# Performance work log

Measured on AMD Instinct MI355X. Metric: run time of the kernel, lower is better.

The kernel has to match this reference:

```python
import jax, jax.numpy as jnp
import numpy as np

NUM_CEPS = 13  # default num_ceps in log_mel_to_cepstral


def _dct_basis(n_mels, num_ceps):
    # Orthonormal DCT-II basis (scipy.fftpack.dct type=2, norm='ortho'),
    # truncated to the first num_ceps rows. Shape (num_ceps, n_mels).
    n = jnp.arange(n_mels, dtype=jnp.float32)
    k = jnp.arange(num_ceps, dtype=jnp.float32)
    basis = jnp.cos(jnp.pi * (n[None, :] + 0.5) * k[:, None] / n_mels)
    scale = jnp.where(k == 0, jnp.sqrt(1.0 / n_mels), jnp.sqrt(2.0 / n_mels))
    return basis * scale[:, None]


def _log_mel_to_cepstral(mel, basis):
    # mel: (B, 1, F, T) -> cepstral (B, num_ceps, T) with CMVN over (B*T)
    x = jnp.log1p(jnp.abs(mel[:, 0]))                 # (B, F, T)
    c = jnp.einsum('kf,bft->bkt', basis, x)           # (B, num_ceps, T)
    mean = jnp.mean(c, axis=(0, 2), keepdims=True)
    # torch .std is unbiased (ddof=1) over the B*T flattened samples
    std = jnp.std(c, axis=(0, 2), keepdims=True, ddof=1) + 1e-6
    return (c - mean) / std


def setup_inputs() -> dict:
    key = jax.random.key(0)
    k1, k2 = jax.random.split(key)
    B, F, T = 64, 128, 4096
    mel_true = jax.random.normal(k1, (B, 1, F, T), dtype=jnp.float32)
    mel_pred = jax.random.normal(k2, (B, 1, F, T), dtype=jnp.float32)
    return {"mel_true": mel_true, "mel_pred": mel_pred}


def reference(mel_true, mel_pred):
    n_mels = mel_true.shape[2]
    basis = _dct_basis(n_mels, NUM_CEPS)
    c_true = _log_mel_to_cepstral(mel_true, basis)
    c_pred = _log_mel_to_cepstral(mel_pred, basis)
    diff = c_true - c_pred
    mse_dist = jnp.sum(diff * diff, axis=1)           # (B, T)
    log_base_10 = 10.0 / jnp.log(jnp.float32(10.0))
    mcd = log_base_10 * jnp.sqrt(2.0 * mse_dist)
    return jnp.mean(mcd)
```

## Files before the change

### kernel.cpp

```cpp
#include <hip/hip_runtime.h>
#include <math.h>

#define BB 64
#define FF 128
#define TT 4096
#define KK 13
#define NT (BB * TT)
#define NP (NT / 2)
#define SCALE0 0.08838834764831845f
#define SCALEK 0.125f
#define MCD_C  6.14185100f

#define KLIST(X) X(0) X(1) X(2) X(3) X(4) X(5) X(6) X(7) X(8) X(9) X(10) X(11) X(12)
#define K12(X)        X(1) X(2) X(3) X(4) X(5) X(6) X(7) X(8) X(9) X(10) X(11) X(12)

__global__ __launch_bounds__(256, 2) void pass1_kernel(
    const float* __restrict__ melT, const float* __restrict__ melP,
    float* __restrict__ sums, float* __restrict__ cT, float* __restrict__ cP)
{
    const int gp = blockIdx.x * 256 + threadIdx.x;
    const int g0 = gp << 1;
    const int b  = g0 >> 12;
    const int t0 = g0 & (TT - 1);
    const float* pT = melT + (size_t)b * FF * TT + t0;
    const float* pP = melP + (size_t)b * FF * TT + t0;

#define DECLACC(i) float tx##i = 0.f, ty##i = 0.f, px##i = 0.f, py##i = 0.f;
    KLIST(DECLACC)

#pragma unroll 4
    for (int f = 0; f < FF; ++f) {
        const float2 vT = *(const float2*)(pT + (size_t)f * TT);
        const float2 vP = *(const float2*)(pP + (size_t)f * TT);
        float xTx = __logf(1.0f + fabsf(vT.x));
        float xTy = __logf(1.0f + fabsf(vT.y));
        float xPx = __logf(1.0f + fabsf(vP.x));
        float xPy = __logf(1.0f + fabsf(vP.y));

        float b1 = __cosf((3.14159265358979f / 128.0f) * ((float)f + 0.5f));
        float tw = b1 + b1;
        float b2  = fmaf(tw, b1,  -1.0f);
        float b3  = fmaf(tw, b2,  -b1);
        float b4  = fmaf(tw, b3,  -b2);
        float b5  = fmaf(tw, b4,  -b3);
        float b6  = fmaf(tw, b5,  -b4);
        float b7  = fmaf(tw, b6,  -b5);
        float b8  = fmaf(tw, b7,  -b6);
        float b9  = fmaf(tw, b8,  -b7);
        float b10 = fmaf(tw, b9,  -b8);
        float b11 = fmaf(tw, b10, -b9);
        float b12 = fmaf(tw, b11, -b10);

        tx0 += xTx; ty0 += xTy; px0 += xPx; py0 += xPy;
#define FMAK(i) tx##i = fmaf(b##i, xTx, tx##i); ty##i = fmaf(b##i, xTy, ty##i); \
                px##i = fmaf(b##i, xPx, px##i); py##i = fmaf(b##i, xPy, py##i);
        K12(FMAK)
#undef FMAK
    }

    tx0 *= SCALE0; ty0 *= SCALE0; px0 *= SCALE0; py0 *= SCALE0;
#define SCK(i) tx##i *= SCALEK; ty##i *= SCALEK; px##i *= SCALEK; py##i *= SCALEK;
    K12(SCK)
#undef SCK

#define STK(i) { ((float2*)(cT + (size_t)(i) * NT))[gp] = make_float2(tx##i, ty##i); \
                 ((float2*)(cP + (size_t)(i) * NT))[gp] = make_float2(px##i, py##i); }
    KLIST(STK)
#undef STK

    __shared__ float red[4][52];
    const int lane = threadIdx.x & 63;
    const int wave = threadIdx.x >> 6;
#define REDK(i) { \
        float s1 = tx##i + ty##i; \
        float s2 = fmaf(tx##i, tx##i, ty##i * ty##i); \
        float s3 = px##i + py##i; \
        float s4 = fmaf(px##i, px##i, py##i * py##i); \
        for (int o = 32; o > 0; o >>= 1) { \
            s1 += __shfl_down(s1, o); s2 += __shfl_down(s2, o); \
            s3 += __shfl_down(s3, o); s4 += __shfl_down(s4, o); } \
        if (lane == 0) { red[wave][i] = s1; red[wave][13 + i] = s2; \
                         red[wave][26 + i] = s3; red[wave][39 + i] = s4; } }
    KLIST(REDK)
#undef REDK
    __syncthreads();
    if (threadIdx.x < 52) {
        atomicAdd(&sums[threadIdx.x],
                  red[0][threadIdx.x] + red[1][threadIdx.x] +
                  red[2][threadIdx.x] + red[3][threadIdx.x]);
    }
}

__global__ __launch_bounds__(256, 2) void pass2_kernel(
    const float* __restrict__ sums, const float* __restrict__ cT,
    const float* __restrict__ cP, float* __restrict__ out)
{
    __shared__ float mT[13], iT[13], mP[13], iP[13];
    if (threadIdx.x < 26) {
        const int arr = threadIdx.x >= 13;
        const int k   = threadIdx.x - arr * 13;
        const float s = sums[arr * 26 + k];
        const float q = sums[arr * 26 + 13 + k];
        const float N = (float)NT;
        const float m = s / N;
        const float var = fmaxf((q - s * m) / (N - 1.0f), 0.0f);
        const float isd = 1.0f / (sqrtf(var) + 1e-6f);
        if (arr == 0) { mT[k] = m; iT[k] = isd; }
        else          { mP[k] = m; iP[k] = isd; }
    }
    __syncthreads();

    const int gp = blockIdx.x * 256 + threadIdx.x;
    float ssx = 0.0f, ssy = 0.0f;
#pragma unroll
    for (int k = 0; k < KK; ++k) {
        const float2 a = ((const float2*)(cT + (size_t)k * NT))[gp];
        const float2 p = ((const float2*)(cP + (size_t)k * NT))[gp];
        const float dx = (a.x - mT[k]) * iT[k] - (p.x - mP[k]) * iP[k];
        const float dy = (a.y - mT[k]) * iT[k] - (p.y - mP[k]) * iP[k];
        ssx = fmaf(dx, dx, ssx);
        ssy = fmaf(dy, dy, ssy);
    }
    float v = MCD_C * (sqrtf(ssx) + sqrtf(ssy));

    const int lane = threadIdx.x & 63;
    const int wave = threadIdx.x >> 6;
    for (int o = 32; o > 0; o >>= 1) v += __shfl_down(v, o);
    __shared__ float r2[4];
    if (lane == 0) r2[wave] = v;
    __syncthreads();
    if (threadIdx.x == 0) {
        atomicAdd(out, (r2[0] + r2[1] + r2[2] + r2[3]) * (1.0f / (float)NT));
    }
}

extern "C" void kernel_launch(void* const* d_in, const int* in_sizes, int n_in,
                              void* d_out, int out_size, void* d_ws, size_t ws_size,
                              hipStream_t stream) {
    const float* melT = (const float*)d_in[0];
    const float* melP = (const float*)d_in[1];
    float* out  = (float*)d_out;
    float* sums = (float*)d_ws;
    float* cT   = (float*)((char*)d_ws + 256);
    float* cP   = cT + (size_t)KK * NT;

    hipMemsetAsync(d_ws, 0, 256, stream);
    hipMemsetAsync(d_out, 0, out_size * sizeof(float), stream);

    pass1_kernel<<<NP / 256, 256, 0, stream>>>(melT, melP, sums, cT, cP);
    pass2_kernel<<<NP / 256, 256, 0, stream>>>(sums, cT, cP, out);
}
```

Before: 296.5 us.

## Split pass1 per tensor, pad atomic sums, replace final atomic with reduce kernel

Pass1 now launches twice as many blocks, each handling only one of the two mel tensors. This halves the accumulator registers per thread and raises the launch-bounds occupancy target from 2 to 4 blocks per SM. The statistic sums are padded to 64-byte spacing to reduce atomic contention on shared cache lines. The final reduction writes per-block partials and adds a third single-block kernel in place of the global atomic, at the cost of an extra launch.

Measured after the change: 291.6 us. Within noise of the previous version (-1.7%).

```diff
diff --git a/kernel.cpp b/kernel.cpp
--- a/kernel.cpp
+++ b/kernel.cpp
@@ -6,106 +6,102 @@
 #define TT 4096
 #define KK 13
 #define NT (BB * TT)
-#define NP (NT / 2)
+#define NPAIR (NT / 2)
 #define SCALE0 0.08838834764831845f
 #define SCALEK 0.125f
 #define MCD_C  6.14185100f
 
+
 #define KLIST(X) X(0) X(1) X(2) X(3) X(4) X(5) X(6) X(7) X(8) X(9) X(10) X(11) X(12)
 #define K12(X)        X(1) X(2) X(3) X(4) X(5) X(6) X(7) X(8) X(9) X(10) X(11) X(12)
 
-__global__ __launch_bounds__(256, 2) void pass1_kernel(
+__global__ __launch_bounds__(256, 4) void pass1_kernel(
     const float* __restrict__ melT, const float* __restrict__ melP,
     float* __restrict__ sums, float* __restrict__ cT, float* __restrict__ cP)
 {
-    const int gp = blockIdx.x * 256 + threadIdx.x;
+    const int tensor = blockIdx.x >> 9;
+    const int gp = ((blockIdx.x & 511) << 8) + threadIdx.x;
+    const float* __restrict__ src = tensor ? melP : melT;
+    float* __restrict__ dst = tensor ? cP : cT;
+
     const int g0 = gp << 1;
     const int b  = g0 >> 12;
     const int t0 = g0 & (TT - 1);
-    const float* pT = melT + (size_t)b * FF * TT + t0;
-    const float* pP = melP + (size_t)b * FF * TT + t0;
+    const float* p = src + (size_t)b * (FF * TT) + t0;
 
-#define DECLACC(i) float tx##i = 0.f, ty##i = 0.f, px##i = 0.f, py##i = 0.f;
+#define DECLACC(i) float ax##i = 0.f, ay##i = 0.f;
     KLIST(DECLACC)
+#undef DECLACC
 
 #pragma unroll 4
     for (int f = 0; f < FF; ++f) {
-        const float2 vT = *(const float2*)(pT + (size_t)f * TT);
-        const float2 vP = *(const float2*)(pP + (size_t)f * TT);
-        float xTx = __logf(1.0f + fabsf(vT.x));
-        float xTy = __logf(1.0f + fabsf(vT.y));
-        float xPx = __logf(1.0f + fabsf(vP.x));
-        float xPy = __logf(1.0f + fabsf(vP.y));
+        const float2 v = *(const float2*)(p + (size_t)f * TT);
+        const float xx = __logf(1.0f + fabsf(v.x));
+        const float xy = __logf(1.0f + fabsf(v.y));
 
-        float b1 = __cosf((3.14159265358979f / 128.0f) * ((float)f + 0.5f));
-        float tw = b1 + b1;
-        float b2  = fmaf(tw, b1,  -1.0f);
-        float b3  = fmaf(tw, b2,  -b1);
-        float b4  = fmaf(tw, b3,  -b2);
-        float b5  = fmaf(tw, b4,  -b3);
-        float b6  = fmaf(tw, b5,  -b4);
-        float b7  = fmaf(tw, b6,  -b5);
-        float b8  = fmaf(tw, b7,  -b6);
-        float b9  = fmaf(tw, b8,  -b7);
-        float b10 = fmaf(tw, b9,  -b8);
-        float b11 = fmaf(tw, b10, -b9);
-        float b12 = fmaf(tw, b11, -b10);
+        const float b1 = __cosf((3.14159265358979f / 128.0f) * ((float)f + 0.5f));
+        const float tw = b1 + b1;
+        const float b2  = fmaf(tw, b1,  -1.0f);
+        const float b3  = fmaf(tw, b2,  -b1);
+        const float b4  = fmaf(tw, b3,  -b2);
+        const float b5  = fmaf(tw, b4,  -b3);
+        const float b6  = fmaf(tw, b5,  -b4);
+        const float b7  = fmaf(tw, b6,  -b5);
+        const float b8  = fmaf(tw, b7,  -b6);
+        const float b9  = fmaf(tw, b8,  -b7);
+        const float b10 = fmaf(tw, b9,  -b8);
+        const float b11 = fmaf(tw, b10, -b9);
+        const float b12 = fmaf(tw, b11, -b10);
 
-        tx0 += xTx; ty0 += xTy; px0 += xPx; py0 += xPy;
-#define FMAK(i) tx##i = fmaf(b##i, xTx, tx##i); ty##i = fmaf(b##i, xTy, ty##i); \
-                px##i = fmaf(b##i, xPx, px##i); py##i = fmaf(b##i, xPy, py##i);
+        ax0 += xx; ay0 += xy;
+#define FMAK(i) ax##i = fmaf(b##i, xx, ax##i); ay##i = fmaf(b##i, xy, ay##i);
         K12(FMAK)
 #undef FMAK
     }
 
-    tx0 *= SCALE0; ty0 *= SCALE0; px0 *= SCALE0; py0 *= SCALE0;
-#define SCK(i) tx##i *= SCALEK; ty##i *= SCALEK; px##i *= SCALEK; py##i *= SCALEK;
+    ax0 *= SCALE0; ay0 *= SCALE0;
+#define SCK(i) ax##i *= SCALEK; ay##i *= SCALEK;
     K12(SCK)
 #undef SCK
 
-#define STK(i) { ((float2*)(cT + (size_t)(i) * NT))[gp] = make_float2(tx##i, ty##i); \
-                 ((float2*)(cP + (size_t)(i) * NT))[gp] = make_float2(px##i, py##i); }
+#define STK(i) ((float2*)(dst + (size_t)(i) * NT))[gp] = make_float2(ax##i, ay##i);
     KLIST(STK)
 #undef STK
 
-    __shared__ float red[4][52];
+    __shared__ float red[4][26];
     const int lane = threadIdx.x & 63;
     const int wave = threadIdx.x >> 6;
 #define REDK(i) { \
-        float s1 = tx##i + ty##i; \
-        float s2 = fmaf(tx##i, tx##i, ty##i * ty##i); \
-        float s3 = px##i + py##i; \
-        float s4 = fmaf(px##i, px##i, py##i * py##i); \
+        float s = ax##i + ay##i; \
+        float q = fmaf(ax##i, ax##i, ay##i * ay##i); \
         for (int o = 32; o > 0; o >>= 1) { \
-            s1 += __shfl_down(s1, o); s2 += __shfl_down(s2, o); \
-            s3 += __shfl_down(s3, o); s4 += __shfl_down(s4, o); } \
-        if (lane == 0) { red[wave][i] = s1; red[wave][13 + i] = s2; \
-                         red[wave][26 + i] = s3; red[wave][39 + i] = s4; } }
+            s += __shfl_down(s, o); q += __shfl_down(q, o); } \
+        if (lane == 0) { red[wave][i] = s; red[wave][13 + i] = q; } }
     KLIST(REDK)
 #undef REDK
     __syncthreads();
-    if (threadIdx.x < 52) {
-        atomicAdd(&sums[threadIdx.x],
-                  red[0][threadIdx.x] + red[1][threadIdx.x] +
-                  red[2][threadIdx.x] + red[3][threadIdx.x]);
+    if (threadIdx.x < 26) {
+        const float v = red[0][threadIdx.x] + red[1][threadIdx.x] +
+                        red[2][threadIdx.x] + red[3][threadIdx.x];
+        atomicAdd(&sums[(tensor * 26 + threadIdx.x) * 16], v);
     }
 }
 
-__global__ __launch_bounds__(256, 2) void pass2_kernel(
+__global__ __launch_bounds__(256, 4) void pass2_kernel(
     const float* __restrict__ sums, const float* __restrict__ cT,
-    const float* __restrict__ cP, float* __restrict__ out)
+    const float* __restrict__ cP, float* __restrict__ partials)
 {
     __shared__ float mT[13], iT[13], mP[13], iP[13];
     if (threadIdx.x < 26) {
-        const int arr = threadIdx.x >= 13;
-        const int k   = threadIdx.x - arr * 13;
-        const float s = sums[arr * 26 + k];
-        const float q = sums[arr * 26 + 13 + k];
+        const int tns = threadIdx.x >= 13;
+        const int k   = threadIdx.x - tns * 13;
+        const float s = sums[(tns * 26 + k) * 16];
+        const float q = sums[(tns * 26 + 13 + k) * 16];
         const float N = (float)NT;
         const float m = s / N;
         const float var = fmaxf((q - s * m) / (N - 1.0f), 0.0f);
         const float isd = 1.0f / (sqrtf(var) + 1e-6f);
-        if (arr == 0) { mT[k] = m; iT[k] = isd; }
+        if (tns == 0) { mT[k] = m; iT[k] = isd; }
         else          { mP[k] = m; iP[k] = isd; }
     }
     __syncthreads();
@@ -129,9 +125,22 @@
     __shared__ float r2[4];
     if (lane == 0) r2[wave] = v;
     __syncthreads();
-    if (threadIdx.x == 0) {
-        atomicAdd(out, (r2[0] + r2[1] + r2[2] + r2[3]) * (1.0f / (float)NT));
-    }
+    if (threadIdx.x == 0)
+        partials[blockIdx.x] = r2[0] + r2[1] + r2[2] + r2[3];
+}
+
+__global__ __launch_bounds__(256) void pass3_kernel(
+    const float* __restrict__ partials, float* __restrict__ out)
+{
+    float v = partials[threadIdx.x] + partials[threadIdx.x + 256];
+    const int lane = threadIdx.x & 63;
+    const int wave = threadIdx.x >> 6;
+    for (int o = 32; o > 0; o >>= 1) v += __shfl_down(v, o);
+    __shared__ float r2[4];
+    if (lane == 0) r2[wave] = v;
+    __syncthreads();
+    if (threadIdx.x == 0)
+        out[0] = (r2[0] + r2[1] + r2[2] + r2[3]) * (1.0f / (float)NT);
 }
 
 extern "C" void kernel_launch(void* const* d_in, const int* in_sizes, int n_in,
@@ -139,14 +148,15 @@
                               hipStream_t stream) {
     const float* melT = (const float*)d_in[0];
     const float* melP = (const float*)d_in[1];
-    float* out  = (float*)d_out;
-    float* sums = (float*)d_ws;
-    float* cT   = (float*)((char*)d_ws + 256);
-    float* cP   = cT + (size_t)KK * NT;
+    float* out      = (float*)d_out;
+    float* sums     = (float*)d_ws;
+    float* partials = (float*)((char*)d_ws + 4096);
+    float* cT       = (float*)((char*)d_ws + 8192);
+    float* cP       = cT + (size_t)KK * NT;
 
-    hipMemsetAsync(d_ws, 0, 256, stream);
-    hipMemsetAsync(d_out, 0, out_size * sizeof(float), stream);
+    hipMemsetAsync(d_ws, 0, 4096, stream);
 
-    pass1_kernel<<<NP / 256, 256, 0, stream>>>(melT, melP, sums, cT, cP);
-    pass2_kernel<<<NP / 256, 256, 0, stream>>>(sums, cT, cP, out);
+    pass1_kernel<<<1024, 256, 0, stream>>>(melT, melP, sums, cT, cP);
+    pass2_kernel<<<512, 256, 0, stream>>>(sums, cT, cP, partials);
+    pass3_kernel<<<1, 256, 0, stream>>>(partials, out);
 }
```
